# Kernel tuning notes

Hardware: AMD Instinct MI355X
Metric: run time of the kernel (lower is better)

Reference implementation:

```python
import jax, jax.numpy as jnp
import numpy as np

VOCAB, EMBED, HIDDEN, NCLASS = 32000, 256, 512, 2
BATCH, SEQ = 64, 512


def setup_inputs() -> dict:
    key = jax.random.key(0)
    ks = jax.random.split(key, 12)
    s_e = 1.0 / np.sqrt(HIDDEN)  # pytorch RNN init scale
    inp = {
        "x": jax.random.randint(ks[0], (BATCH, SEQ), 0, VOCAB),
        "emb": jax.random.normal(ks[1], (VOCAB, EMBED), dtype=jnp.float32),
        "W_ih0": jax.random.uniform(ks[2], (HIDDEN, EMBED), minval=-s_e, maxval=s_e),
        "W_hh0": jax.random.uniform(ks[3], (HIDDEN, HIDDEN), minval=-s_e, maxval=s_e),
        "b_ih0": jax.random.uniform(ks[4], (HIDDEN,), minval=-s_e, maxval=s_e),
        "b_hh0": jax.random.uniform(ks[5], (HIDDEN,), minval=-s_e, maxval=s_e),
        "W_ih1": jax.random.uniform(ks[6], (HIDDEN, HIDDEN), minval=-s_e, maxval=s_e),
        "W_hh1": jax.random.uniform(ks[7], (HIDDEN, HIDDEN), minval=-s_e, maxval=s_e),
        "b_ih1": jax.random.uniform(ks[8], (HIDDEN,), minval=-s_e, maxval=s_e),
        "b_hh1": jax.random.uniform(ks[9], (HIDDEN,), minval=-s_e, maxval=s_e),
        "W_out": jax.random.uniform(ks[10], (NCLASS, HIDDEN), minval=-s_e, maxval=s_e),
        "b_out": jax.random.uniform(ks[11], (NCLASS,), minval=-s_e, maxval=s_e),
    }
    return inp


def _rnn_layer(inp_bse, W_ih, W_hh, b_ih, b_hh):
    """Vanilla tanh RNN layer. inp: [B,S,E] -> out: [B,S,H]."""
    # precompute input projection for all timesteps (one big GEMM)
    xp = jnp.einsum("bse,he->bsh", inp_bse, W_ih) + b_ih + b_hh  # [B,S,H]
    B = inp_bse.shape[0]
    h0 = jnp.zeros((B, W_hh.shape[0]), dtype=inp_bse.dtype)

    def step(h, xp_t):
        h = jnp.tanh(xp_t + h @ W_hh.T)
        return h, h

    _, out = jax.lax.scan(step, h0, jnp.swapaxes(xp, 0, 1))  # out: [S,B,H]
    return jnp.swapaxes(out, 0, 1)


def reference(x, emb, W_ih0, W_hh0, b_ih0, b_hh0, W_ih1, W_hh1, b_ih1, b_hh1,
              W_out, b_out):
    h = emb[x]  # [B,S,E] embedding lookup
    h = _rnn_layer(h, W_ih0, W_hh0, b_ih0, b_hh0)  # layer 1
    h = _rnn_layer(h, W_ih1, W_hh1, b_ih1, b_hh1)  # layer 2
    pooled = jnp.mean(h, axis=1)  # avg_pool2d over (S,1) == mean over time -> [B,H]
    return pooled @ W_out.T + b_out  # [B,2]
```

## Files before the change

### kernel.cpp

```cpp
#include <hip/hip_runtime.h>
#include <math.h>

#define BB 64
#define SS 512
#define EE 256
#define HH 512

#define NGROUPS 16
#define GSLICES 8
#define LBLK 16
#define BPG 4
#define RECT 512


__global__ void transpose512(const float* __restrict__ in, float* __restrict__ out) {
  __shared__ float tile[32][33];
  int bx = blockIdx.x * 32, by = blockIdx.y * 32;
  int x = threadIdx.x, y0 = threadIdx.y;
  for (int dy = 0; dy < 32; dy += 8)
    tile[y0 + dy][x] = in[(size_t)(by + y0 + dy) * HH + bx + x];
  __syncthreads();
  for (int dy = 0; dy < 32; dy += 8)
    out[(size_t)(bx + y0 + dy) * HH + by + x] = tile[x][y0 + dy];
}

template <int K, bool GATHER>
__global__ __launch_bounds__(256) void xp_gemm(
    const float* __restrict__ Asrc, const int* __restrict__ xidx,
    const float* __restrict__ emb, const float* __restrict__ Wn,
    const float* __restrict__ bias1, const float* __restrict__ bias2,
    float* __restrict__ C) {
  const int tid = threadIdx.x;
  const int m0 = blockIdx.x * 64;
  const int n0 = blockIdx.y * 64;
  __shared__ alignas(16) float As[32][68];
  __shared__ alignas(16) float Bs[32][68];
  __shared__ int xs[64];
  if (GATHER) {
    if (tid < 64) xs[tid] = xidx[m0 + tid];
    __syncthreads();
  }
  float acc[4][4] = {};
  const int ty = tid >> 4, tx = tid & 15;
  const int row = tid >> 2;
  const int kc = (tid & 3) * 8;

  for (int k0 = 0; k0 < K; k0 += 32) {
    const float* ap;
    if (GATHER) ap = emb + (size_t)xs[row] * EE + (k0 + kc);
    else        ap = Asrc + (size_t)(m0 + row) * K + (k0 + kc);
    float4 av0 = *(const float4*)ap;
    float4 av1 = *(const float4*)(ap + 4);
    const float* bp = Wn + (size_t)(n0 + row) * K + (k0 + kc);
    float4 bv0 = *(const float4*)bp;
    float4 bv1 = *(const float4*)(bp + 4);
    __syncthreads();
    As[kc + 0][row] = av0.x; As[kc + 1][row] = av0.y;
    As[kc + 2][row] = av0.z; As[kc + 3][row] = av0.w;
    As[kc + 4][row] = av1.x; As[kc + 5][row] = av1.y;
    As[kc + 6][row] = av1.z; As[kc + 7][row] = av1.w;
    Bs[kc + 0][row] = bv0.x; Bs[kc + 1][row] = bv0.y;
    Bs[kc + 2][row] = bv0.z; Bs[kc + 3][row] = bv0.w;
    Bs[kc + 4][row] = bv1.x; Bs[kc + 5][row] = bv1.y;
    Bs[kc + 6][row] = bv1.z; Bs[kc + 7][row] = bv1.w;
    __syncthreads();
#pragma unroll 8
    for (int k = 0; k < 32; ++k) {
      float4 av = *(const float4*)&As[k][ty * 4];
      float4 bv = *(const float4*)&Bs[k][tx * 4];
      acc[0][0] += av.x * bv.x; acc[0][1] += av.x * bv.y;
      acc[0][2] += av.x * bv.z; acc[0][3] += av.x * bv.w;
      acc[1][0] += av.y * bv.x; acc[1][1] += av.y * bv.y;
      acc[1][2] += av.y * bv.z; acc[1][3] += av.y * bv.w;
      acc[2][0] += av.z * bv.x; acc[2][1] += av.z * bv.y;
      acc[2][2] += av.z * bv.z; acc[2][3] += av.z * bv.w;
      acc[3][0] += av.w * bv.x; acc[3][1] += av.w * bv.y;
      acc[3][2] += av.w * bv.z; acc[3][3] += av.w * bv.w;
    }
  }
  float bj[4];
#pragma unroll
  for (int j = 0; j < 4; ++j) {
    int n = n0 + tx * 4 + j;
    bj[j] = bias1[n] + bias2[n];
  }
#pragma unroll
  for (int i = 0; i < 4; ++i) {
    float4 cv = make_float4(acc[i][0] + bj[0], acc[i][1] + bj[1],
                            acc[i][2] + bj[2], acc[i][3] + bj[3]);
    *(float4*)&C[(size_t)(m0 + ty * 4 + i) * HH + n0 + tx * 4] = cv;
  }
}

__global__ void init_sync(float* __restrict__ h0b, float* __restrict__ h1b,
                          unsigned* __restrict__ flags) {
  int i = blockIdx.x * 256 + threadIdx.x;
  if (i < NGROUPS * 2 * BPG * HH) {
    __hip_atomic_store(&h0b[i], 0.f, __ATOMIC_RELAXED, __HIP_MEMORY_SCOPE_SYSTEM);
    __hip_atomic_store(&h1b[i], 0.f, __ATOMIC_RELAXED, __HIP_MEMORY_SCOPE_SYSTEM);
  }
  if (i < NGROUPS * LBLK * 4 * 32)
    __hip_atomic_store(&flags[i], 0u, __ATOMIC_RELAXED, __HIP_MEMORY_SCOPE_SYSTEM);
}

__device__ __forceinline__ void fma4(float4& d, const float4 w, const float s) {
  d.x = __builtin_fmaf(w.x, s, d.x);
  d.y = __builtin_fmaf(w.y, s, d.y);
  d.z = __builtin_fmaf(w.z, s, d.z);
  d.w = __builtin_fmaf(w.w, s, d.w);
}

__device__ __forceinline__ float4 ic_ld4(const float* p) {
  float4 v;
  asm volatile("global_load_dwordx4 %0, %1, off sc0 sc1" : "=v"(v) : "v"(p));
  return v;
}

__device__ __forceinline__ void fma_mv_lds(float4 acc[4], const float4 wreg[16],
                                           const float* h, int jg) {
#pragma unroll
  for (int q = 0; q < 4; ++q) {
    float4 w0 = wreg[q * 4 + 0], w1 = wreg[q * 4 + 1];
    float4 w2 = wreg[q * 4 + 2], w3 = wreg[q * 4 + 3];
#pragma unroll
    for (int b = 0; b < 4; ++b) {
      float4 hv = *(const float4*)&h[b * HH + jg * 16 + q * 4];
      fma4(acc[b], w0, hv.x);
      fma4(acc[b], w1, hv.y);
      fma4(acc[b], w2, hv.z);
      fma4(acc[b], w3, hv.w);
    }
  }
}

__device__ __forceinline__ void ld_h16(float4 hr[4][4], const float* hp0) {
  const float* hp2 = hp0 + 2 * HH;
  asm volatile(
    "global_load_dwordx4 %0, %4, off sc0 sc1\n\t"
    "global_load_dwordx4 %1, %4, off offset:16 sc0 sc1\n\t"
    "global_load_dwordx4 %2, %4, off offset:32 sc0 sc1\n\t"
    "global_load_dwordx4 %3, %4, off offset:48 sc0 sc1"
    : "=&v"(hr[0][0]), "=&v"(hr[0][1]), "=&v"(hr[0][2]), "=&v"(hr[0][3])
    : "v"(hp0));
  asm volatile(
    "global_load_dwordx4 %0, %4, off offset:2048 sc0 sc1\n\t"
    "global_load_dwordx4 %1, %4, off offset:2064 sc0 sc1\n\t"
    "global_load_dwordx4 %2, %4, off offset:2080 sc0 sc1\n\t"
    "global_load_dwordx4 %3, %4, off offset:2096 sc0 sc1"
    : "=&v"(hr[1][0]), "=&v"(hr[1][1]), "=&v"(hr[1][2]), "=&v"(hr[1][3])
    : "v"(hp0));
  asm volatile(
    "global_load_dwordx4 %0, %4, off sc0 sc1\n\t"
    "global_load_dwordx4 %1, %4, off offset:16 sc0 sc1\n\t"
    "global_load_dwordx4 %2, %4, off offset:32 sc0 sc1\n\t"
    "global_load_dwordx4 %3, %4, off offset:48 sc0 sc1"
    : "=&v"(hr[2][0]), "=&v"(hr[2][1]), "=&v"(hr[2][2]), "=&v"(hr[2][3])
    : "v"(hp2));
  asm volatile(
    "global_load_dwordx4 %0, %4, off offset:2048 sc0 sc1\n\t"
    "global_load_dwordx4 %1, %4, off offset:2064 sc0 sc1\n\t"
    "global_load_dwordx4 %2, %4, off offset:2080 sc0 sc1\n\t"
    "global_load_dwordx4 %3, %4, off offset:2096 sc0 sc1"
    : "=&v"(hr[3][0]), "=&v"(hr[3][1]), "=&v"(hr[3][2]), "=&v"(hr[3][3])
    : "v"(hp2));
}

__device__ __forceinline__ void fma_mv(float4 acc[4], const float4 wreg[16],
                                       const float4 hr[4][4]) {
#pragma unroll
  for (int q = 0; q < 4; ++q) {
    float4 w0 = wreg[q * 4 + 0], w1 = wreg[q * 4 + 1];
    float4 w2 = wreg[q * 4 + 2], w3 = wreg[q * 4 + 3];
#pragma unroll
    for (int b = 0; b < 4; ++b) {
      float4 hv = hr[b][q];
      fma4(acc[b], w0, hv.x);
      fma4(acc[b], w1, hv.y);
      fma4(acc[b], w2, hv.z);
      fma4(acc[b], w3, hv.w);
    }
  }
}

__global__ __launch_bounds__(RECT, 2) void rec_fused(
    const float* __restrict__ xp,
    const float* __restrict__ WThh0,
    const float* __restrict__ WTih1,
    const float* __restrict__ WThh1,
    const float* __restrict__ b_ih1,
    const float* __restrict__ b_hh1,
    float* __restrict__ pooled,
    float* __restrict__ h0b,
    float* __restrict__ h1b,
    unsigned* __restrict__ flags) {
  const int tid = threadIdx.x;
  const int bid = blockIdx.x;
  const int grp = bid & 15;
  const int role = bid >> 4;
  const bool isL1 = role >= GSLICES;
  const int slice = role & 7;
  const int oo4 = tid & 15;
  const int jg = tid >> 4;
  const int obase = slice * 64 + oo4 * 4;

  float4 wregA[16], wregB[16];
  {
    const float* wb = isL1 ? WThh1 : WThh0;
#pragma unroll
    for (int j = 0; j < 16; ++j)
      wregB[j] = *(const float4*)&wb[(size_t)(jg * 16 + j) * HH + obase];
#pragma unroll
    for (int j = 0; j < 16; ++j)
      asm volatile("" : "+v"(wregB[j].x), "+v"(wregB[j].y),
                        "+v"(wregB[j].z), "+v"(wregB[j].w));
  }
  if (isL1) {
#pragma unroll
    for (int j = 0; j < 16; ++j)
      wregA[j] = *(const float4*)&WTih1[(size_t)(jg * 16 + j) * HH + obase];
#pragma unroll
    for (int j = 0; j < 16; ++j)
      asm volatile("" : "+v"(wregA[j].x), "+v"(wregA[j].y),
                        "+v"(wregA[j].z), "+v"(wregA[j].w));
  }

  float* h0g = h0b + (size_t)grp * (2 * BPG * HH);
  float* h1g = h1b + (size_t)grp * (2 * BPG * HH);
  unsigned* flg = flags + (size_t)grp * (LBLK * 4 * 32);

  __shared__ alignas(16) float hA[BPG * HH];
  __shared__ alignas(16) float hB[BPG * HH];
  __shared__ float part[8][16][17];

  const int wave = tid >> 6, wl = tid & 63;
  const int fo = tid & 63;
  const int fbb = (tid >> 6) & 3;
  const int fog = slice * 64 + fo;
  const size_t fxbase = (size_t)(grp * BPG + fbb) * (SS * HH) + fog;
  float pacc = 0.f;
  float bs = 0.f;
  if (tid < 256) bs = b_ih1[fog] + b_hh1[fog];

  for (int s = 0; s < SS; ++s) {
    const bool doC = (!isL1) || (s >= 1);
    float4 acc[BPG] = {{0,0,0,0},{0,0,0,0},{0,0,0,0},{0,0,0,0}};
    float xv = 0.f;
    if (doC) {
      const float* srcA;
      const float* srcB = nullptr;
      if (!isL1) {
        srcA = h0g + (size_t)((s + 1) & 1) * (BPG * HH);
      } else {
        srcA = h0g + (size_t)((s - 1) & 1) * (BPG * HH);
        srcB = h1g + (size_t)(s & 1) * (BPG * HH);
      }
      float4 va = ic_ld4(srcA + tid * 4);
      float4 vb;
      if (isL1) vb = ic_ld4(srcB + tid * 4);
      if (!isL1 && tid < 256) xv = xp[fxbase + (size_t)s * HH];
      asm volatile("s_waitcnt vmcnt(0)" ::: "memory");
      __builtin_amdgcn_sched_barrier(0);
      *(float4*)&hA[tid * 4] = va;
      if (isL1) *(float4*)&hB[tid * 4] = vb;
      __syncthreads();

      if (!isL1) {
        fma_mv_lds(acc, wregB, hA, jg);
      } else {
        fma_mv_lds(acc, wregA, hA, jg);
        fma_mv_lds(acc, wregB, hB, jg);
      }

#pragma unroll
      for (int b = 0; b < BPG; ++b) {
        acc[b].x += __shfl_down(acc[b].x, 32); acc[b].y += __shfl_down(acc[b].y, 32);
        acc[b].z += __shfl_down(acc[b].z, 32); acc[b].w += __shfl_down(acc[b].w, 32);
        acc[b].x += __shfl_down(acc[b].x, 16); acc[b].y += __shfl_down(acc[b].y, 16);
        acc[b].z += __shfl_down(acc[b].z, 16); acc[b].w += __shfl_down(acc[b].w, 16);
      }
      if (wl < 16) {
#pragma unroll
        for (int b = 0; b < BPG; ++b) {
          part[wave][wl][b * 4 + 0] = acc[b].x;
          part[wave][wl][b * 4 + 1] = acc[b].y;
          part[wave][wl][b * 4 + 2] = acc[b].z;
          part[wave][wl][b * 4 + 3] = acc[b].w;
        }
      }
    }
    __syncthreads();

    if (tid < 256) {
      if (doC) {
        float v = isL1 ? bs : xv;
#pragma unroll
        for (int w = 0; w < 8; ++w) v += part[w][fo >> 2][fbb * 4 + (fo & 3)];
        float h = tanhf(v);
        float* hst;
        if (!isL1)
          hst = h0g + ((size_t)(s & 1) * BPG + fbb) * HH + fog;
        else {
          hst = h1g + ((size_t)((s - 1) & 1) * BPG + fbb) * HH + fog;
          pacc += h;
        }
        asm volatile("global_store_dword %0, %1, off sc0 sc1"
                     :: "v"(hst), "v"(h) : "memory");
      }
      asm volatile("s_waitcnt vmcnt(0)" ::: "memory");
      if (wl == 0) {
        unsigned tp1 = (unsigned)(s + 1);
        unsigned* sf = flg + ((role << 2) + wave) * 32;
        asm volatile("global_store_dword %0, %1, off sc0 sc1"
                     :: "v"(sf), "v"(tp1) : "memory");
      }
    }

    if (tid < 64) {
      const unsigned tp1 = (unsigned)(s + 1);
      unsigned* fp = flg + tid * 32;
      unsigned v;
      do {
        asm volatile("global_load_dword %0, %1, off sc0 sc1\n\t"
                     "s_waitcnt vmcnt(0)"
                     : "=v"(v) : "v"(fp) : "memory");
      } while (v < tp1);
    }
    __syncthreads();
  }

  if (isL1) {
    float4 acc[BPG] = {{0,0,0,0},{0,0,0,0},{0,0,0,0},{0,0,0,0}};
    float4 hr[4][4];
    ld_h16(hr, h0g + (size_t)1 * (BPG * HH) + jg * 16);
    asm volatile("s_waitcnt vmcnt(0)" ::: "memory");
    __builtin_amdgcn_sched_barrier(0);
    fma_mv(acc, wregA, hr);
    ld_h16(hr, h1g + jg * 16);
    asm volatile("s_waitcnt vmcnt(0)" ::: "memory");
    __builtin_amdgcn_sched_barrier(0);
    fma_mv(acc, wregB, hr);
#pragma unroll
    for (int b = 0; b < BPG; ++b) {
      acc[b].x += __shfl_down(acc[b].x, 32); acc[b].y += __shfl_down(acc[b].y, 32);
      acc[b].z += __shfl_down(acc[b].z, 32); acc[b].w += __shfl_down(acc[b].w, 32);
      acc[b].x += __shfl_down(acc[b].x, 16); acc[b].y += __shfl_down(acc[b].y, 16);
      acc[b].z += __shfl_down(acc[b].z, 16); acc[b].w += __shfl_down(acc[b].w, 16);
    }
    if (wl < 16) {
#pragma unroll
      for (int b = 0; b < BPG; ++b) {
        part[wave][wl][b * 4 + 0] = acc[b].x;
        part[wave][wl][b * 4 + 1] = acc[b].y;
        part[wave][wl][b * 4 + 2] = acc[b].z;
        part[wave][wl][b * 4 + 3] = acc[b].w;
      }
    }
    __syncthreads();
    if (tid < 256) {
      float v = bs;
#pragma unroll
      for (int w = 0; w < 8; ++w) v += part[w][fo >> 2][fbb * 4 + (fo & 3)];
      pacc += tanhf(v);
      pooled[(size_t)(grp * BPG + fbb) * HH + fog] = pacc * (1.0f / SS);
    }
  }
}

__global__ void out_kernel(const float* __restrict__ pooled,
                           const float* __restrict__ W_out,
                           const float* __restrict__ b_out,
                           float* __restrict__ out) {
  int tid = threadIdx.x;
  if (tid >= BB * 2) return;
  int b = tid >> 1, c = tid & 1;
  float acc = b_out[c];
  for (int k = 0; k < HH; ++k)
    acc += pooled[(size_t)b * HH + k] * W_out[(size_t)c * HH + k];
  out[(size_t)b * 2 + c] = acc;
}

extern "C" void kernel_launch(void* const* d_in, const int* in_sizes, int n_in,
                              void* d_out, int out_size, void* d_ws, size_t ws_size,
                              hipStream_t stream) {
  const int*   x     = (const int*)d_in[0];
  const float* emb   = (const float*)d_in[1];
  const float* W_ih0 = (const float*)d_in[2];
  const float* W_hh0 = (const float*)d_in[3];
  const float* b_ih0 = (const float*)d_in[4];
  const float* b_hh0 = (const float*)d_in[5];
  const float* W_ih1 = (const float*)d_in[6];
  const float* W_hh1 = (const float*)d_in[7];
  const float* b_ih1 = (const float*)d_in[8];
  const float* b_hh1 = (const float*)d_in[9];
  const float* W_out = (const float*)d_in[10];
  const float* b_out = (const float*)d_in[11];

  float* ws = (float*)d_ws;
  const size_t NBSH = (size_t)BB * SS * HH;
  const size_t HB   = (size_t)NGROUPS * 2 * BPG * HH;
  const size_t FL   = (size_t)NGROUPS * LBLK * 4 * 32;
  float* xp      = ws;
  float* WThh0   = ws + NBSH;
  float* WTih1   = WThh0 + HH * HH;
  float* WThh1   = WTih1 + HH * HH;
  float* pooled  = WThh1 + HH * HH;
  float* h0buf   = pooled + BB * HH;
  float* h1buf   = h0buf + HB;
  unsigned* flags = (unsigned*)(h1buf + HB);

  init_sync<<<512, 256, 0, stream>>>(h0buf, h1buf, flags);

  dim3 tb(32, 8), tg(16, 16);
  transpose512<<<tg, tb, 0, stream>>>(W_hh0, WThh0);
  transpose512<<<tg, tb, 0, stream>>>(W_ih1, WTih1);
  transpose512<<<tg, tb, 0, stream>>>(W_hh1, WThh1);

  dim3 gg(512, 8);
  xp_gemm<EE, true><<<gg, 256, 0, stream>>>(nullptr, x, emb, W_ih0, b_ih0, b_hh0, xp);
  rec_fused<<<NGROUPS * LBLK, RECT, 0, stream>>>(
      xp, WThh0, WTih1, WThh1, b_ih1, b_hh1, pooled, h0buf, h1buf, flags);
  out_kernel<<<1, 128, 0, stream>>>(pooled, W_out, b_out, (float*)d_out);
}
```

Before: 2.034 ms.

## Replace per-step flag barriers with tagged hidden-state packets in a ring buffer

```diff
diff --git a/kernel.cpp b/kernel.cpp
--- a/kernel.cpp
+++ b/kernel.cpp
@@ -11,6 +11,11 @@
 #define LBLK 16
 #define BPG 4
 #define RECT 512
+#define RING 16
+#define BARK 8
+
+#define SLOTF (GSLICES * 512)
+#define GPKF  (2 * RING * SLOTF)
 
 
 __global__ void transpose512(const float* __restrict__ in, float* __restrict__ out) {
@@ -92,14 +97,11 @@
   }
 }
 
-__global__ void init_sync(float* __restrict__ h0b, float* __restrict__ h1b,
-                          unsigned* __restrict__ flags) {
-  int i = blockIdx.x * 256 + threadIdx.x;
-  if (i < NGROUPS * 2 * BPG * HH) {
-    __hip_atomic_store(&h0b[i], 0.f, __ATOMIC_RELAXED, __HIP_MEMORY_SCOPE_SYSTEM);
-    __hip_atomic_store(&h1b[i], 0.f, __ATOMIC_RELAXED, __HIP_MEMORY_SCOPE_SYSTEM);
-  }
-  if (i < NGROUPS * LBLK * 4 * 32)
+__global__ void init_sync(float* __restrict__ pkts, unsigned* __restrict__ flags) {
+  size_t i = (size_t)blockIdx.x * 256 + threadIdx.x;
+  if (i < (size_t)NGROUPS * GPKF)
+    __hip_atomic_store(&pkts[i], 0.f, __ATOMIC_RELAXED, __HIP_MEMORY_SCOPE_SYSTEM);
+  if (i < NGROUPS * LBLK * 32)
     __hip_atomic_store(&flags[i], 0u, __ATOMIC_RELAXED, __HIP_MEMORY_SCOPE_SYSTEM);
 }
 
@@ -110,10 +112,45 @@
   d.w = __builtin_fmaf(w.w, s, d.w);
 }
 
-__device__ __forceinline__ float4 ic_ld4(const float* p) {
-  float4 v;
-  asm volatile("global_load_dwordx4 %0, %1, off sc0 sc1" : "=v"(v) : "v"(p));
-  return v;
+__device__ __forceinline__ void poll2(const float* pb, unsigned tg,
+                                      float4& u0, float4& u1) {
+  for (;;) {
+    asm volatile(
+      "global_load_dwordx4 %0, %2, off sc0 sc1\n\t"
+      "global_load_dwordx4 %1, %2, off offset:16 sc0 sc1\n\t"
+      "s_waitcnt vmcnt(0)"
+      : "=&v"(u0), "=&v"(u1) : "v"(pb) : "memory");
+    if (__float_as_uint(u0.y) == tg && __float_as_uint(u0.w) == tg &&
+        __float_as_uint(u1.y) == tg && __float_as_uint(u1.w) == tg) break;
+    __builtin_amdgcn_s_sleep(1);
+  }
+}
+
+__device__ __forceinline__ void poll4(const float* pa, unsigned tga,
+                                      const float* pb, unsigned tgb,
+                                      float4& a0, float4& a1,
+                                      float4& b0, float4& b1) {
+  for (;;) {
+    asm volatile(
+      "global_load_dwordx4 %0, %4, off sc0 sc1\n\t"
+      "global_load_dwordx4 %1, %4, off offset:16 sc0 sc1\n\t"
+      "global_load_dwordx4 %2, %5, off sc0 sc1\n\t"
+      "global_load_dwordx4 %3, %5, off offset:16 sc0 sc1\n\t"
+      "s_waitcnt vmcnt(0)"
+      : "=&v"(a0), "=&v"(a1), "=&v"(b0), "=&v"(b1)
+      : "v"(pa), "v"(pb) : "memory");
+    if (__float_as_uint(a0.y) == tga && __float_as_uint(a0.w) == tga &&
+        __float_as_uint(a1.y) == tga && __float_as_uint(a1.w) == tga &&
+        __float_as_uint(b0.y) == tgb && __float_as_uint(b0.w) == tgb &&
+        __float_as_uint(b1.y) == tgb && __float_as_uint(b1.w) == tgb) break;
+    __builtin_amdgcn_s_sleep(1);
+  }
+}
+
+__device__ __forceinline__ void scat(float* hs, int q0, float4 u0, float4 u1) {
+  int b = (q0 >> 6) & 3;
+  int j0 = (q0 >> 8) * 64 + (q0 & 63);
+  *(float4*)&hs[b * HH + j0] = make_float4(u0.x, u0.z, u1.x, u1.z);
 }
 
 __device__ __forceinline__ void fma_mv_lds(float4 acc[4], const float4 wreg[16],
@@ -125,55 +162,6 @@
 #pragma unroll
     for (int b = 0; b < 4; ++b) {
       float4 hv = *(const float4*)&h[b * HH + jg * 16 + q * 4];
-      fma4(acc[b], w0, hv.x);
-      fma4(acc[b], w1, hv.y);
-      fma4(acc[b], w2, hv.z);
-      fma4(acc[b], w3, hv.w);
-    }
-  }
-}
-
-__device__ __forceinline__ void ld_h16(float4 hr[4][4], const float* hp0) {
-  const float* hp2 = hp0 + 2 * HH;
-  asm volatile(
-    "global_load_dwordx4 %0, %4, off sc0 sc1\n\t"
-    "global_load_dwordx4 %1, %4, off offset:16 sc0 sc1\n\t"
-    "global_load_dwordx4 %2, %4, off offset:32 sc0 sc1\n\t"
-    "global_load_dwordx4 %3, %4, off offset:48 sc0 sc1"
-    : "=&v"(hr[0][0]), "=&v"(hr[0][1]), "=&v"(hr[0][2]), "=&v"(hr[0][3])
-    : "v"(hp0));
-  asm volatile(
-    "global_load_dwordx4 %0, %4, off offset:2048 sc0 sc1\n\t"
-    "global_load_dwordx4 %1, %4, off offset:2064 sc0 sc1\n\t"
-    "global_load_dwordx4 %2, %4, off offset:2080 sc0 sc1\n\t"
-    "global_load_dwordx4 %3, %4, off offset:2096 sc0 sc1"
-    : "=&v"(hr[1][0]), "=&v"(hr[1][1]), "=&v"(hr[1][2]), "=&v"(hr[1][3])
-    : "v"(hp0));
-  asm volatile(
-    "global_load_dwordx4 %0, %4, off sc0 sc1\n\t"
-    "global_load_dwordx4 %1, %4, off offset:16 sc0 sc1\n\t"
-    "global_load_dwordx4 %2, %4, off offset:32 sc0 sc1\n\t"
-    "global_load_dwordx4 %3, %4, off offset:48 sc0 sc1"
-    : "=&v"(hr[2][0]), "=&v"(hr[2][1]), "=&v"(hr[2][2]), "=&v"(hr[2][3])
-    : "v"(hp2));
-  asm volatile(
-    "global_load_dwordx4 %0, %4, off offset:2048 sc0 sc1\n\t"
-    "global_load_dwordx4 %1, %4, off offset:2064 sc0 sc1\n\t"
-    "global_load_dwordx4 %2, %4, off offset:2080 sc0 sc1\n\t"
-    "global_load_dwordx4 %3, %4, off offset:2096 sc0 sc1"
-    : "=&v"(hr[3][0]), "=&v"(hr[3][1]), "=&v"(hr[3][2]), "=&v"(hr[3][3])
-    : "v"(hp2));
-}
-
-__device__ __forceinline__ void fma_mv(float4 acc[4], const float4 wreg[16],
-                                       const float4 hr[4][4]) {
-#pragma unroll
-  for (int q = 0; q < 4; ++q) {
-    float4 w0 = wreg[q * 4 + 0], w1 = wreg[q * 4 + 1];
-    float4 w2 = wreg[q * 4 + 2], w3 = wreg[q * 4 + 3];
-#pragma unroll
-    for (int b = 0; b < 4; ++b) {
-      float4 hv = hr[b][q];
       fma4(acc[b], w0, hv.x);
       fma4(acc[b], w1, hv.y);
       fma4(acc[b], w2, hv.z);
@@ -190,8 +178,7 @@
     const float* __restrict__ b_ih1,
     const float* __restrict__ b_hh1,
     float* __restrict__ pooled,
-    float* __restrict__ h0b,
-    float* __restrict__ h1b,
+    float* __restrict__ pkts,
     unsigned* __restrict__ flags) {
   const int tid = threadIdx.x;
   const int bid = blockIdx.x;
@@ -224,9 +211,8 @@
                         "+v"(wregA[j].z), "+v"(wregA[j].w));
   }
 
-  float* h0g = h0b + (size_t)grp * (2 * BPG * HH);
-  float* h1g = h1b + (size_t)grp * (2 * BPG * HH);
-  unsigned* flg = flags + (size_t)grp * (LBLK * 4 * 32);
+  float* pk = pkts + (size_t)grp * GPKF;
+  unsigned* flg = flags + grp * (LBLK * 32);
 
   __shared__ alignas(16) float hA[BPG * HH];
   __shared__ alignas(16) float hB[BPG * HH];
@@ -241,36 +227,45 @@
   float bs = 0.f;
   if (tid < 256) bs = b_ih1[fog] + b_hh1[fog];
 
+  const int q0 = tid * 4;
+  const int toff = tid * 8;
+  const int wpo = slice * 512 + (fbb * 64 + fo) * 2;
+
   for (int s = 0; s < SS; ++s) {
-    const bool doC = (!isL1) || (s >= 1);
+    float xv = 0.f;
+    if (!isL1) {
+      if (tid < 256) xv = xp[fxbase + (size_t)s * HH];
+      if (s >= 1) {
+        float4 u0, u1;
+        const float* pb = pk + (size_t)((s - 1) & 15) * SLOTF + toff;
+        poll2(pb, (unsigned)s, u0, u1);
+        scat(hA, q0, u0, u1);
+      }
+    } else {
+      if (s >= 2) {
+        float4 a0, a1, b0, b1;
+        const float* pa = pk + (size_t)((s - 1) & 15) * SLOTF + toff;
+        const float* pb = pk + (size_t)(RING + ((s - 2) & 15)) * SLOTF + toff;
+        poll4(pa, (unsigned)s, pb, (unsigned)(s - 1), a0, a1, b0, b1);
+        scat(hA, q0, a0, a1);
+        scat(hB, q0, b0, b1);
+      } else if (s == 1) {
+        float4 a0, a1;
+        const float* pa = pk + (size_t)0 * SLOTF + toff;
+        poll2(pa, 1u, a0, a1);
+        scat(hA, q0, a0, a1);
+      }
+    }
+    __syncthreads();
+
     float4 acc[BPG] = {{0,0,0,0},{0,0,0,0},{0,0,0,0},{0,0,0,0}};
-    float xv = 0.f;
-    if (doC) {
-      const float* srcA;
-      const float* srcB = nullptr;
-      if (!isL1) {
-        srcA = h0g + (size_t)((s + 1) & 1) * (BPG * HH);
-      } else {
-        srcA = h0g + (size_t)((s - 1) & 1) * (BPG * HH);
-        srcB = h1g + (size_t)(s & 1) * (BPG * HH);
-      }
-      float4 va = ic_ld4(srcA + tid * 4);
-      float4 vb;
-      if (isL1) vb = ic_ld4(srcB + tid * 4);
-      if (!isL1 && tid < 256) xv = xp[fxbase + (size_t)s * HH];
-      asm volatile("s_waitcnt vmcnt(0)" ::: "memory");
-      __builtin_amdgcn_sched_barrier(0);
-      *(float4*)&hA[tid * 4] = va;
-      if (isL1) *(float4*)&hB[tid * 4] = vb;
-      __syncthreads();
-
+    if (s >= 1) {
       if (!isL1) {
         fma_mv_lds(acc, wregB, hA, jg);
       } else {
         fma_mv_lds(acc, wregA, hA, jg);
-        fma_mv_lds(acc, wregB, hB, jg);
-      }
-
+        if (s >= 2) fma_mv_lds(acc, wregB, hB, jg);
+      }
 #pragma unroll
       for (int b = 0; b < BPG; ++b) {
         acc[b].x += __shfl_down(acc[b].x, 32); acc[b].y += __shfl_down(acc[b].y, 32);
@@ -291,54 +286,61 @@
     __syncthreads();
 
     if (tid < 256) {
-      if (doC) {
-        float v = isL1 ? bs : xv;
+      if (!isL1) {
+        float v = xv;
+        if (s >= 1) {
+#pragma unroll
+          for (int w = 0; w < 8; ++w) v += part[w][fo >> 2][fbb * 4 + (fo & 3)];
+        }
+        float h = tanhf(v);
+        float* pw = pk + (size_t)(s & 15) * SLOTF + wpo;
+        float2 pkt; pkt.x = h; pkt.y = __uint_as_float((unsigned)(s + 1));
+        asm volatile("global_store_dwordx2 %0, %1, off sc0 sc1"
+                     :: "v"(pw), "v"(pkt) : "memory");
+      } else if (s >= 1) {
+        float v = bs;
 #pragma unroll
         for (int w = 0; w < 8; ++w) v += part[w][fo >> 2][fbb * 4 + (fo & 3)];
         float h = tanhf(v);
-        float* hst;
-        if (!isL1)
-          hst = h0g + ((size_t)(s & 1) * BPG + fbb) * HH + fog;
-        else {
-          hst = h1g + ((size_t)((s - 1) & 1) * BPG + fbb) * HH + fog;
-          pacc += h;
-        }
+        pacc += h;
+        float* pw = pk + (size_t)(RING + ((s - 1) & 15)) * SLOTF + wpo;
+        float2 pkt; pkt.x = h; pkt.y = __uint_as_float((unsigned)s);
+        asm volatile("global_store_dwordx2 %0, %1, off sc0 sc1"
+                     :: "v"(pw), "v"(pkt) : "memory");
+      }
+    }
+
+    if ((s & (BARK - 1)) == (BARK - 1)) {
+      unsigned bt = (unsigned)((s >> 3) + 1);
+      if (tid == 0) {
+        unsigned* fp = flg + role * 32;
         asm volatile("global_store_dword %0, %1, off sc0 sc1"
-                     :: "v"(hst), "v"(h) : "memory");
-      }
-      asm volatile("s_waitcnt vmcnt(0)" ::: "memory");
-      if (wl == 0) {
-        unsigned tp1 = (unsigned)(s + 1);
-        unsigned* sf = flg + ((role << 2) + wave) * 32;
-        asm volatile("global_store_dword %0, %1, off sc0 sc1"
-                     :: "v"(sf), "v"(tp1) : "memory");
-      }
-    }
-
-    if (tid < 64) {
-      const unsigned tp1 = (unsigned)(s + 1);
-      unsigned* fp = flg + tid * 32;
-      unsigned v;
-      do {
-        asm volatile("global_load_dword %0, %1, off sc0 sc1\n\t"
-                     "s_waitcnt vmcnt(0)"
-                     : "=v"(v) : "v"(fp) : "memory");
-      } while (v < tp1);
-    }
-    __syncthreads();
+                     :: "v"(fp), "v"(bt) : "memory");
+      }
+      if (tid < LBLK) {
+        const unsigned* fp = flg + tid * 32;
+        unsigned v;
+        do {
+          asm volatile("global_load_dword %0, %1, off sc0 sc1\n\ts_waitcnt vmcnt(0)"
+                       : "=v"(v) : "v"(fp) : "memory");
+          if (v < bt) __builtin_amdgcn_s_sleep(2);
+        } while (v < bt);
+      }
+      __syncthreads();
+    }
   }
 
   if (isL1) {
+    float4 a0, a1, b0, b1;
+    const float* pa = pk + (size_t)15 * SLOTF + toff;
+    const float* pb = pk + (size_t)(RING + 14) * SLOTF + toff;
+    poll4(pa, (unsigned)SS, pb, (unsigned)(SS - 1), a0, a1, b0, b1);
+    scat(hA, q0, a0, a1);
+    scat(hB, q0, b0, b1);
+    __syncthreads();
     float4 acc[BPG] = {{0,0,0,0},{0,0,0,0},{0,0,0,0},{0,0,0,0}};
-    float4 hr[4][4];
-    ld_h16(hr, h0g + (size_t)1 * (BPG * HH) + jg * 16);
-    asm volatile("s_waitcnt vmcnt(0)" ::: "memory");
-    __builtin_amdgcn_sched_barrier(0);
-    fma_mv(acc, wregA, hr);
-    ld_h16(hr, h1g + jg * 16);
-    asm volatile("s_waitcnt vmcnt(0)" ::: "memory");
-    __builtin_amdgcn_sched_barrier(0);
-    fma_mv(acc, wregB, hr);
+    fma_mv_lds(acc, wregA, hA, jg);
+    fma_mv_lds(acc, wregB, hB, jg);
 #pragma unroll
     for (int b = 0; b < BPG; ++b) {
       acc[b].x += __shfl_down(acc[b].x, 32); acc[b].y += __shfl_down(acc[b].y, 32);
@@ -397,18 +399,16 @@
 
   float* ws = (float*)d_ws;
   const size_t NBSH = (size_t)BB * SS * HH;
-  const size_t HB   = (size_t)NGROUPS * 2 * BPG * HH;
-  const size_t FL   = (size_t)NGROUPS * LBLK * 4 * 32;
+  const size_t PKF  = (size_t)NGROUPS * GPKF;
   float* xp      = ws;
   float* WThh0   = ws + NBSH;
   float* WTih1   = WThh0 + HH * HH;
   float* WThh1   = WTih1 + HH * HH;
   float* pooled  = WThh1 + HH * HH;
-  float* h0buf   = pooled + BB * HH;
-  float* h1buf   = h0buf + HB;
-  unsigned* flags = (unsigned*)(h1buf + HB);
-
-  init_sync<<<512, 256, 0, stream>>>(h0buf, h1buf, flags);
+  float* pkts    = pooled + BB * HH;
+  unsigned* flags = (unsigned*)(pkts + PKF);
+
+  init_sync<<<8192, 256, 0, stream>>>(pkts, flags);
 
   dim3 tb(32, 8), tg(16, 16);
   transpose512<<<tg, tb, 0, stream>>>(W_hh0, WThh0);
@@ -418,6 +418,6 @@
   dim3 gg(512, 8);
   xp_gemm<EE, true><<<gg, 256, 0, stream>>>(nullptr, x, emb, W_ih0, b_ih0, b_hh0, xp);
   rec_fused<<<NGROUPS * LBLK, RECT, 0, stream>>>(
-      xp, WThh0, WTih1, WThh1, b_ih1, b_hh1, pooled, h0buf, h1buf, flags);
+      xp, WThh0, WTih1, WThh1, b_ih1, b_hh1, pooled, pkts, flags);
   out_kernel<<<1, 128, 0, stream>>>(pooled, W_out, b_out, (float*)d_out);
 }
```

Result: no change. 2.034 ms (-0.0%).
